# Optimization experiments

Measured on AMD Instinct MI355X. Metric: run time of the kernel, lower is better.

## Reference

```python
import jax, jax.numpy as jnp
import numpy as np

HEADS = 4

def setup_inputs() -> dict:
    B, L, D = 4, 2048, 256
    key = jax.random.key(0)
    k1, k2, k3, k4, k5, k6 = jax.random.split(key, 6)
    return {
        "atten": jax.random.normal(k1, (B, L, L), dtype=jnp.float32),
        "value": jax.random.normal(k2, (B, L, D), dtype=jnp.float32),
        "mask": jax.random.uniform(k3, (B, 1, L, L), dtype=jnp.float32),
        "padding_mask": jax.random.randint(k4, (B, L, L), 0, 2, dtype=jnp.int32),
        "Wv": jax.random.normal(k5, (D, D), dtype=jnp.float32) * 0.02,
        "bv": jnp.zeros((D,), dtype=jnp.float32),
        "Wo": jax.random.normal(k6, (D, D), dtype=jnp.float32) * 0.02,
        "bo": jnp.zeros((D,), dtype=jnp.float32),
    }

def reference(atten, value, mask, padding_mask, Wv, bv, Wo, bo):
    B, L, D = value.shape
    H = HEADS
    dk = D // H
    # to_value: Linear then split heads. N == 1 (value.unsqueeze(1) in torch).
    v = value @ Wv + bv                                   # (B, L, D)
    v = v.reshape(B, 1, L, H, dk).transpose(0, 3, 1, 2, 4)  # (B, H, N=1, L, dk)
    # externally supplied attention logits, two sequential masked fills
    a = atten[:, None, :, :]                              # (B, 1, L, L)
    a = jnp.where(mask < 0.5, jnp.finfo(a.dtype).min, a)
    a = jnp.where(padding_mask[:, None, :, :] == 0, -jnp.inf, a)
    a = jax.nn.softmax(a, axis=-1)                        # (B, 1, L, L)
    # dropout is identity in eval mode
    # einsum 'bhij,bhnjk->bhnik' with h=1 on a broadcast across H heads of v
    out = jnp.einsum('bij,bhnjk->bhnik', a[:, 0], v)      # (B, H, 1, L, dk)
    out = out.transpose(0, 2, 3, 1, 4).reshape(B, 1, L, D)
    out = out @ Wo + bo                                   # (B, 1, L, D)
    return out
```

## Files before the change

### kernel.cpp

```cpp
#include <hip/hip_runtime.h>
#include <hip/hip_bf16.h>
#include <math.h>

#define L 2048
#define D 256

typedef __attribute__((ext_vector_type(8))) short bf16x8;
typedef __attribute__((ext_vector_type(4))) float f32x4;
typedef __attribute__((ext_vector_type(4))) int i32x4;

__device__ __forceinline__ unsigned short f2bf(float f) {
    union { float f; unsigned int u; } v; v.f = f;
    unsigned int r = v.u + 0x7FFFu + ((v.u >> 16) & 1u);
    return (unsigned short)(r >> 16);
}

__global__ __launch_bounds__(256) void wtrans_kernel(
    const float* __restrict__ Wv, const float* __restrict__ Wo,
    unsigned short* __restrict__ Wvt, unsigned short* __restrict__ Wot) {
    int idx = blockIdx.x * 256 + threadIdx.x;
    int which = idx >> 16;
    int e = idx & 65535;
    int n = e >> 8, k = e & 255;
    const float* W = which ? Wo : Wv;
    unsigned short* Wt = which ? Wot : Wvt;
    Wt[n * 256 + k] = f2bf(W[k * 256 + n]);
}

__global__ __launch_bounds__(256) void gemm_v_kernel(
    const float* __restrict__ A,
    const unsigned short* __restrict__ Wt,
    const float* __restrict__ bias,
    unsigned short* __restrict__ Vt) {
    const int wave = threadIdx.x >> 6;
    const int lane = threadIdx.x & 63;
    const int mh = wave >> 1, nh = wave & 1;
    const int lm = lane & 15, q = lane >> 4;
    const int m0 = blockIdx.x * 64;
    const int n0 = blockIdx.y * 128;

    f32x4 acc[2][4];
#pragma unroll
    for (int i = 0; i < 2; i++)
#pragma unroll
        for (int j = 0; j < 4; j++) acc[i][j] = (f32x4)(0.f);

    int arow[2];
    arow[0] = m0 + mh * 32 + lm;
    arow[1] = arow[0] + 16;
    int ncol[4];
#pragma unroll
    for (int nf = 0; nf < 4; nf++) ncol[nf] = n0 + nh * 64 + nf * 16 + lm;

    for (int k0 = 0; k0 < 256; k0 += 32) {
        int kq = k0 + q * 8;
        bf16x8 bfr[4];
#pragma unroll
        for (int nf = 0; nf < 4; nf++)
            bfr[nf] = *reinterpret_cast<const bf16x8*>(Wt + ncol[nf] * 256 + kq);
        bf16x8 afr[2];
#pragma unroll
        for (int mf = 0; mf < 2; mf++) {
            const float* ap = A + arow[mf] * 256 + kq;
            f32x4 a0 = *reinterpret_cast<const f32x4*>(ap);
            f32x4 a1 = *reinterpret_cast<const f32x4*>(ap + 4);
            bf16x8 t;
#pragma unroll
            for (int e = 0; e < 4; e++) t[e] = (short)f2bf(a0[e]);
#pragma unroll
            for (int e = 0; e < 4; e++) t[4 + e] = (short)f2bf(a1[e]);
            afr[mf] = t;
        }
#pragma unroll
        for (int mf = 0; mf < 2; mf++)
#pragma unroll
            for (int nf = 0; nf < 4; nf++)
                acc[mf][nf] = __builtin_amdgcn_mfma_f32_16x16x32_bf16(
                    afr[mf], bfr[nf], acc[mf][nf], 0, 0, 0);
    }

#pragma unroll
    for (int mf = 0; mf < 2; mf++) {
        int mrow = m0 + mh * 32 + mf * 16 + q * 4;
#pragma unroll
        for (int nf = 0; nf < 4; nf++) {
            int n = ncol[nf];
            float bias_n = bias[n];
            int b = mrow >> 11;
            int j = mrow & 2047;
            unsigned short* dst = Vt + (size_t)b * (D * L) + (size_t)n * L + j;
            ushort4 pk;
            pk.x = f2bf(acc[mf][nf][0] + bias_n);
            pk.y = f2bf(acc[mf][nf][1] + bias_n);
            pk.z = f2bf(acc[mf][nf][2] + bias_n);
            pk.w = f2bf(acc[mf][nf][3] + bias_n);
            *reinterpret_cast<ushort4*>(dst) = pk;
        }
    }
}

__global__ __launch_bounds__(256) void p_kernel(
    const float* __restrict__ atten, const float* __restrict__ mask,
    const int* __restrict__ pad, unsigned short* __restrict__ P,
    float* __restrict__ lsum) {
    const int row = blockIdx.x * 4 + (threadIdx.x >> 6);
    const int lane = threadIdx.x & 63;

    const float* at = atten + (size_t)row * L;
    const float* mk = mask  + (size_t)row * L;
    const int*   pd = pad   + (size_t)row * L;
    unsigned short* Pr = P + (size_t)row * L;

    float l_th = 0.f;
#pragma unroll
    for (int c = 0; c < 8; c++) {
        const int off = c * 256 + lane * 4;
        f32x4 a = *reinterpret_cast<const f32x4*>(at + off);
        f32x4 m = *reinterpret_cast<const f32x4*>(mk + off);
        i32x4 p = *reinterpret_cast<const i32x4*>(pd + off);
        ushort4 pk;
        float pv;
        pv = (m[0] < 0.5f || p[0] == 0) ? 0.f : __expf(a[0]); l_th += pv; pk.x = f2bf(pv);
        pv = (m[1] < 0.5f || p[1] == 0) ? 0.f : __expf(a[1]); l_th += pv; pk.y = f2bf(pv);
        pv = (m[2] < 0.5f || p[2] == 0) ? 0.f : __expf(a[2]); l_th += pv; pk.z = f2bf(pv);
        pv = (m[3] < 0.5f || p[3] == 0) ? 0.f : __expf(a[3]); l_th += pv; pk.w = f2bf(pv);
        *reinterpret_cast<ushort4*>(Pr + off) = pk;
    }
#pragma unroll
    for (int off = 1; off < 64; off <<= 1) l_th += __shfl_xor(l_th, off);
    if (lane == 0) lsum[row] = l_th;
}

__global__ __launch_bounds__(256) void pv_out_kernel(
    const unsigned short* __restrict__ P, const unsigned short* __restrict__ Vt,
    const float* __restrict__ lsum, const unsigned short* __restrict__ Wot,
    const float* __restrict__ bo, float* __restrict__ out) {
    const int rb = blockIdx.x;
    const int tid = threadIdx.x;
    const int w = tid >> 6, lane = tid & 63;
    const int lm = lane & 15, q = lane >> 4;
    const int b = rb >> 6;
    const int row0 = rb * 32;

    const unsigned short* pA = P + (size_t)row0 * L + q * 8;
    const unsigned short* pB = Vt + (size_t)b * (D * L) + (size_t)(w * 64) * L + q * 8;

    f32x4 acc[2][4];
#pragma unroll
    for (int i = 0; i < 2; i++)
#pragma unroll
        for (int j = 0; j < 4; j++) acc[i][j] = (f32x4)(0.f);

    bf16x8 Ac[2][2], Bc[2][4], An[2][2], Bn[2][4];
#pragma unroll
    for (int kk = 0; kk < 2; kk++) {
#pragma unroll
        for (int mf = 0; mf < 2; mf++)
            Ac[kk][mf] = *reinterpret_cast<const bf16x8*>(pA + (mf * 16 + lm) * L + kk * 32);
#pragma unroll
        for (int nf = 0; nf < 4; nf++)
            Bc[kk][nf] = *reinterpret_cast<const bf16x8*>(pB + (nf * 16 + lm) * L + kk * 32);
    }

    for (int k0 = 0; k0 < 2048; k0 += 64) {
        if (k0 + 64 < 2048) {
            const int kn = k0 + 64;
#pragma unroll
            for (int kk = 0; kk < 2; kk++) {
#pragma unroll
                for (int mf = 0; mf < 2; mf++)
                    An[kk][mf] = *reinterpret_cast<const bf16x8*>(
                        pA + (mf * 16 + lm) * L + kn + kk * 32);
#pragma unroll
                for (int nf = 0; nf < 4; nf++)
                    Bn[kk][nf] = *reinterpret_cast<const bf16x8*>(
                        pB + (nf * 16 + lm) * L + kn + kk * 32);
            }
        }
#pragma unroll
        for (int kk = 0; kk < 2; kk++)
#pragma unroll
            for (int mf = 0; mf < 2; mf++)
#pragma unroll
                for (int nf = 0; nf < 4; nf++)
                    acc[mf][nf] = __builtin_amdgcn_mfma_f32_16x16x32_bf16(
                        Ac[kk][mf], Bc[kk][nf], acc[mf][nf], 0, 0, 0);
#pragma unroll
        for (int kk = 0; kk < 2; kk++) {
#pragma unroll
            for (int mf = 0; mf < 2; mf++) Ac[kk][mf] = An[kk][mf];
#pragma unroll
            for (int nf = 0; nf < 4; nf++) Bc[kk][nf] = Bn[kk][nf];
        }
    }

    __shared__ __align__(16) unsigned short Alds[32][264];
#pragma unroll
    for (int mf = 0; mf < 2; mf++) {
        float inv[4];
#pragma unroll
        for (int rg = 0; rg < 4; rg++)
            inv[rg] = 1.f / lsum[row0 + mf * 16 + q * 4 + rg];
#pragma unroll
        for (int nf = 0; nf < 4; nf++) {
            int col = w * 64 + nf * 16 + lm;
#pragma unroll
            for (int rg = 0; rg < 4; rg++)
                Alds[mf * 16 + q * 4 + rg][col] = f2bf(acc[mf][nf][rg] * inv[rg]);
        }
    }
    __syncthreads();

    f32x4 oacc[2][4];
#pragma unroll
    for (int i = 0; i < 2; i++)
#pragma unroll
        for (int j = 0; j < 4; j++) oacc[i][j] = (f32x4)(0.f);
    int ncol[4];
#pragma unroll
    for (int nf = 0; nf < 4; nf++) ncol[nf] = w * 64 + nf * 16 + lm;

    for (int kk = 0; kk < 8; kk++) {
        int kq = kk * 32 + q * 8;
        bf16x8 bfr[4];
#pragma unroll
        for (int nf = 0; nf < 4; nf++)
            bfr[nf] = *reinterpret_cast<const bf16x8*>(Wot + ncol[nf] * 256 + kq);
#pragma unroll
        for (int mf = 0; mf < 2; mf++) {
            bf16x8 afr = *reinterpret_cast<const bf16x8*>(&Alds[mf * 16 + lm][kq]);
#pragma unroll
            for (int nf = 0; nf < 4; nf++)
                oacc[mf][nf] = __builtin_amdgcn_mfma_f32_16x16x32_bf16(
                    afr, bfr[nf], oacc[mf][nf], 0, 0, 0);
        }
    }

#pragma unroll
    for (int mf = 0; mf < 2; mf++) {
        int mrow = row0 + mf * 16 + q * 4;
#pragma unroll
        for (int nf = 0; nf < 4; nf++) {
            int n = ncol[nf];
            float bn = bo[n];
#pragma unroll
            for (int rg = 0; rg < 4; rg++)
                out[(size_t)(mrow + rg) * 256 + n] = oacc[mf][nf][rg] + bn;
        }
    }
}

extern "C" void kernel_launch(void* const* d_in, const int* in_sizes, int n_in,
                              void* d_out, int out_size, void* d_ws, size_t ws_size,
                              hipStream_t stream) {
    (void)in_sizes; (void)n_in; (void)out_size; (void)ws_size;
    const float* atten = (const float*)d_in[0];
    const float* value = (const float*)d_in[1];
    const float* mask  = (const float*)d_in[2];
    const int*   pad   = (const int*)d_in[3];
    const float* Wv    = (const float*)d_in[4];
    const float* bv    = (const float*)d_in[5];
    const float* Wo    = (const float*)d_in[6];
    const float* bo    = (const float*)d_in[7];
    float* out = (float*)d_out;

    char* ws = (char*)d_ws;
    unsigned short* Vt  = (unsigned short*)(ws);
    unsigned short* Wvt = (unsigned short*)(ws + 4194304);
    unsigned short* Wot = (unsigned short*)(ws + 4325376);
    unsigned short* P   = (unsigned short*)(ws + 4456448);
    float* lsum         = (float*)(ws + 38010880);

    wtrans_kernel<<<512, 256, 0, stream>>>(Wv, Wo, Wvt, Wot);
    gemm_v_kernel<<<dim3(128, 2), 256, 0, stream>>>(value, Wvt, bv, Vt);
    p_kernel<<<2048, 256, 0, stream>>>(atten, mask, pad, P, lsum);
    pv_out_kernel<<<256, 256, 0, stream>>>(P, Vt, lsum, Wot, bo, out);
}
```

Before: 279.5 us.

## Split PV matmul over K into partial sums with separate combine+output GEMM

The P·V kernel is split four ways along the key dimension, so 1024 blocks run instead of 256. Each block writes fp32 partial sums to workspace, and a new combine kernel sums them, normalises by the row sums, and applies the Wo projection. The p_kernel now gives each wave half a row and prefetches the next chunk, producing two partial row sums. This trades better GPU occupancy for an extra kernel launch and roughly 32MB of partial-sum traffic through global memory.

```diff
diff --git a/kernel.cpp b/kernel.cpp
--- a/kernel.cpp
+++ b/kernel.cpp
@@ -102,48 +102,59 @@
 __global__ __launch_bounds__(256) void p_kernel(
     const float* __restrict__ atten, const float* __restrict__ mask,
     const int* __restrict__ pad, unsigned short* __restrict__ P,
-    float* __restrict__ lsum) {
-    const int row = blockIdx.x * 4 + (threadIdx.x >> 6);
+    float* __restrict__ lsum2) {
+    const int wid = blockIdx.x * 4 + (threadIdx.x >> 6);
+    const int row = wid >> 1, h = wid & 1;
     const int lane = threadIdx.x & 63;
 
-    const float* at = atten + (size_t)row * L;
-    const float* mk = mask  + (size_t)row * L;
-    const int*   pd = pad   + (size_t)row * L;
-    unsigned short* Pr = P + (size_t)row * L;
+    const size_t base = (size_t)row * L + h * 1024 + lane * 4;
+    const float* at = atten + base;
+    const float* mk = mask  + base;
+    const int*   pd = pad   + base;
+    unsigned short* Pr = P + base;
+
+    f32x4 a0 = *reinterpret_cast<const f32x4*>(at);
+    f32x4 m0 = *reinterpret_cast<const f32x4*>(mk);
+    i32x4 p0 = *reinterpret_cast<const i32x4*>(pd);
 
     float l_th = 0.f;
 #pragma unroll
-    for (int c = 0; c < 8; c++) {
-        const int off = c * 256 + lane * 4;
-        f32x4 a = *reinterpret_cast<const f32x4*>(at + off);
-        f32x4 m = *reinterpret_cast<const f32x4*>(mk + off);
-        i32x4 p = *reinterpret_cast<const i32x4*>(pd + off);
+    for (int c = 0; c < 4; c++) {
+        f32x4 a1, m1; i32x4 p1;
+        if (c < 3) {
+            const int off = (c + 1) * 256;
+            a1 = *reinterpret_cast<const f32x4*>(at + off);
+            m1 = *reinterpret_cast<const f32x4*>(mk + off);
+            p1 = *reinterpret_cast<const i32x4*>(pd + off);
+        }
         ushort4 pk;
         float pv;
-        pv = (m[0] < 0.5f || p[0] == 0) ? 0.f : __expf(a[0]); l_th += pv; pk.x = f2bf(pv);
-        pv = (m[1] < 0.5f || p[1] == 0) ? 0.f : __expf(a[1]); l_th += pv; pk.y = f2bf(pv);
-        pv = (m[2] < 0.5f || p[2] == 0) ? 0.f : __expf(a[2]); l_th += pv; pk.z = f2bf(pv);
-        pv = (m[3] < 0.5f || p[3] == 0) ? 0.f : __expf(a[3]); l_th += pv; pk.w = f2bf(pv);
-        *reinterpret_cast<ushort4*>(Pr + off) = pk;
+        pv = (m0[0] < 0.5f || p0[0] == 0) ? 0.f : __expf(a0[0]); l_th += pv; pk.x = f2bf(pv);
+        pv = (m0[1] < 0.5f || p0[1] == 0) ? 0.f : __expf(a0[1]); l_th += pv; pk.y = f2bf(pv);
+        pv = (m0[2] < 0.5f || p0[2] == 0) ? 0.f : __expf(a0[2]); l_th += pv; pk.z = f2bf(pv);
+        pv = (m0[3] < 0.5f || p0[3] == 0) ? 0.f : __expf(a0[3]); l_th += pv; pk.w = f2bf(pv);
+        *reinterpret_cast<ushort4*>(Pr + c * 256) = pk;
+        a0 = a1; m0 = m1; p0 = p1;
     }
 #pragma unroll
     for (int off = 1; off < 64; off <<= 1) l_th += __shfl_xor(l_th, off);
-    if (lane == 0) lsum[row] = l_th;
-}
-
-__global__ __launch_bounds__(256) void pv_out_kernel(
+    if (lane == 0) lsum2[wid] = l_th;
+}
+
+__global__ __launch_bounds__(256) void pv_split_kernel(
     const unsigned short* __restrict__ P, const unsigned short* __restrict__ Vt,
-    const float* __restrict__ lsum, const unsigned short* __restrict__ Wot,
-    const float* __restrict__ bo, float* __restrict__ out) {
+    float* __restrict__ part) {
     const int rb = blockIdx.x;
+    const int sk = blockIdx.y;
     const int tid = threadIdx.x;
     const int w = tid >> 6, lane = tid & 63;
     const int lm = lane & 15, q = lane >> 4;
     const int b = rb >> 6;
     const int row0 = rb * 32;
 
-    const unsigned short* pA = P + (size_t)row0 * L + q * 8;
-    const unsigned short* pB = Vt + (size_t)b * (D * L) + (size_t)(w * 64) * L + q * 8;
+    const unsigned short* pA = P + (size_t)row0 * L + sk * 512 + q * 8;
+    const unsigned short* pB = Vt + (size_t)b * (D * L) + (size_t)(w * 64) * L
+                             + sk * 512 + q * 8;
 
     f32x4 acc[2][4];
 #pragma unroll
@@ -151,71 +162,85 @@
 #pragma unroll
         for (int j = 0; j < 4; j++) acc[i][j] = (f32x4)(0.f);
 
-    bf16x8 Ac[2][2], Bc[2][4], An[2][2], Bn[2][4];
-#pragma unroll
-    for (int kk = 0; kk < 2; kk++) {
+    bf16x8 Ac[2], Bc[4], An[2], Bn[4];
+#pragma unroll
+    for (int mf = 0; mf < 2; mf++)
+        Ac[mf] = *reinterpret_cast<const bf16x8*>(pA + (mf * 16 + lm) * L);
+#pragma unroll
+    for (int nf = 0; nf < 4; nf++)
+        Bc[nf] = *reinterpret_cast<const bf16x8*>(pB + (nf * 16 + lm) * L);
+
+    for (int t = 0; t < 16; t++) {
+        if (t < 15) {
+            const int kn = (t + 1) * 32;
+#pragma unroll
+            for (int mf = 0; mf < 2; mf++)
+                An[mf] = *reinterpret_cast<const bf16x8*>(pA + (mf * 16 + lm) * L + kn);
+#pragma unroll
+            for (int nf = 0; nf < 4; nf++)
+                Bn[nf] = *reinterpret_cast<const bf16x8*>(pB + (nf * 16 + lm) * L + kn);
+        }
 #pragma unroll
         for (int mf = 0; mf < 2; mf++)
-            Ac[kk][mf] = *reinterpret_cast<const bf16x8*>(pA + (mf * 16 + lm) * L + kk * 32);
-#pragma unroll
-        for (int nf = 0; nf < 4; nf++)
-            Bc[kk][nf] = *reinterpret_cast<const bf16x8*>(pB + (nf * 16 + lm) * L + kk * 32);
-    }
-
-    for (int k0 = 0; k0 < 2048; k0 += 64) {
-        if (k0 + 64 < 2048) {
-            const int kn = k0 + 64;
-#pragma unroll
-            for (int kk = 0; kk < 2; kk++) {
-#pragma unroll
-                for (int mf = 0; mf < 2; mf++)
-                    An[kk][mf] = *reinterpret_cast<const bf16x8*>(
-                        pA + (mf * 16 + lm) * L + kn + kk * 32);
-#pragma unroll
-                for (int nf = 0; nf < 4; nf++)
-                    Bn[kk][nf] = *reinterpret_cast<const bf16x8*>(
-                        pB + (nf * 16 + lm) * L + kn + kk * 32);
-            }
-        }
-#pragma unroll
-        for (int kk = 0; kk < 2; kk++)
-#pragma unroll
-            for (int mf = 0; mf < 2; mf++)
-#pragma unroll
-                for (int nf = 0; nf < 4; nf++)
-                    acc[mf][nf] = __builtin_amdgcn_mfma_f32_16x16x32_bf16(
-                        Ac[kk][mf], Bc[kk][nf], acc[mf][nf], 0, 0, 0);
-#pragma unroll
-        for (int kk = 0; kk < 2; kk++) {
-#pragma unroll
-            for (int mf = 0; mf < 2; mf++) Ac[kk][mf] = An[kk][mf];
-#pragma unroll
-            for (int nf = 0; nf < 4; nf++) Bc[kk][nf] = Bn[kk][nf];
-        }
-    }
-
-    __shared__ __align__(16) unsigned short Alds[32][264];
-#pragma unroll
-    for (int mf = 0; mf < 2; mf++) {
-        float inv[4];
-#pragma unroll
-        for (int rg = 0; rg < 4; rg++)
-            inv[rg] = 1.f / lsum[row0 + mf * 16 + q * 4 + rg];
+#pragma unroll
+            for (int nf = 0; nf < 4; nf++)
+                acc[mf][nf] = __builtin_amdgcn_mfma_f32_16x16x32_bf16(
+                    Ac[mf], Bc[nf], acc[mf][nf], 0, 0, 0);
+#pragma unroll
+        for (int mf = 0; mf < 2; mf++) Ac[mf] = An[mf];
+#pragma unroll
+        for (int nf = 0; nf < 4; nf++) Bc[nf] = Bn[nf];
+    }
+
+    float* pb = part + ((size_t)sk * 256 + rb) * (32 * 256);
+#pragma unroll
+    for (int mf = 0; mf < 2; mf++)
 #pragma unroll
         for (int nf = 0; nf < 4; nf++) {
             int col = w * 64 + nf * 16 + lm;
 #pragma unroll
             for (int rg = 0; rg < 4; rg++)
-                Alds[mf * 16 + q * 4 + rg][col] = f2bf(acc[mf][nf][rg] * inv[rg]);
+                pb[(mf * 16 + q * 4 + rg) * 256 + col] = acc[mf][nf][rg];
+        }
+}
+
+__global__ __launch_bounds__(256) void combine_gemm_kernel(
+    const float* __restrict__ part, const float* __restrict__ lsum2,
+    const unsigned short* __restrict__ Wot, const float* __restrict__ bo,
+    float* __restrict__ out) {
+    const int cb = blockIdx.x;
+    const int tid = threadIdx.x;
+    const int w = tid >> 6, lane = tid & 63;
+    const int lm = lane & 15, q = lane >> 4;
+    const int rb = cb >> 1;
+    const int rlo = (cb & 1) * 16;
+
+    __shared__ __align__(16) unsigned short Alds[16][264];
+
+    {
+        const int r16 = tid >> 4;
+        const int c0 = (tid & 15) * 16;
+        const int g = cb * 16 + r16;
+        float l = lsum2[2 * g] + lsum2[2 * g + 1];
+        float inv = 1.f / l;
+        const float* pb = part + (size_t)rb * (32 * 256) + (rlo + r16) * 256 + c0;
+#pragma unroll
+        for (int e = 0; e < 16; e += 4) {
+            f32x4 s = (f32x4)(0.f);
+#pragma unroll
+            for (int skp = 0; skp < 4; skp++)
+                s += *reinterpret_cast<const f32x4*>(pb + (size_t)skp * (256 * 32 * 256) + e);
+            s *= inv;
+            ushort4 pk;
+            pk.x = f2bf(s[0]); pk.y = f2bf(s[1]); pk.z = f2bf(s[2]); pk.w = f2bf(s[3]);
+            *reinterpret_cast<ushort4*>(&Alds[r16][c0 + e]) = pk;
         }
     }
     __syncthreads();
 
-    f32x4 oacc[2][4];
-#pragma unroll
-    for (int i = 0; i < 2; i++)
-#pragma unroll
-        for (int j = 0; j < 4; j++) oacc[i][j] = (f32x4)(0.f);
+    f32x4 oacc[4];
+#pragma unroll
+    for (int j = 0; j < 4; j++) oacc[j] = (f32x4)(0.f);
     int ncol[4];
 #pragma unroll
     for (int nf = 0; nf < 4; nf++) ncol[nf] = w * 64 + nf * 16 + lm;
@@ -226,27 +251,21 @@
 #pragma unroll
         for (int nf = 0; nf < 4; nf++)
             bfr[nf] = *reinterpret_cast<const bf16x8*>(Wot + ncol[nf] * 256 + kq);
-#pragma unroll
-        for (int mf = 0; mf < 2; mf++) {
-            bf16x8 afr = *reinterpret_cast<const bf16x8*>(&Alds[mf * 16 + lm][kq]);
-#pragma unroll
-            for (int nf = 0; nf < 4; nf++)
-                oacc[mf][nf] = __builtin_amdgcn_mfma_f32_16x16x32_bf16(
-                    afr, bfr[nf], oacc[mf][nf], 0, 0, 0);
-        }
-    }
-
-#pragma unroll
-    for (int mf = 0; mf < 2; mf++) {
-        int mrow = row0 + mf * 16 + q * 4;
-#pragma unroll
-        for (int nf = 0; nf < 4; nf++) {
-            int n = ncol[nf];
-            float bn = bo[n];
-#pragma unroll
-            for (int rg = 0; rg < 4; rg++)
-                out[(size_t)(mrow + rg) * 256 + n] = oacc[mf][nf][rg] + bn;
-        }
+        bf16x8 afr = *reinterpret_cast<const bf16x8*>(&Alds[lm][kq]);
+#pragma unroll
+        for (int nf = 0; nf < 4; nf++)
+            oacc[nf] = __builtin_amdgcn_mfma_f32_16x16x32_bf16(
+                afr, bfr[nf], oacc[nf], 0, 0, 0);
+    }
+
+    const int mrow = cb * 16 + q * 4;
+#pragma unroll
+    for (int nf = 0; nf < 4; nf++) {
+        int n = ncol[nf];
+        float bn = bo[n];
+#pragma unroll
+        for (int rg = 0; rg < 4; rg++)
+            out[(size_t)(mrow + rg) * 256 + n] = oacc[nf][rg] + bn;
     }
 }
 
@@ -269,10 +288,12 @@
     unsigned short* Wvt = (unsigned short*)(ws + 4194304);
     unsigned short* Wot = (unsigned short*)(ws + 4325376);
     unsigned short* P   = (unsigned short*)(ws + 4456448);
-    float* lsum         = (float*)(ws + 38010880);
+    float* lsum2        = (float*)(ws + 38010880);
+    float* part         = (float*)(ws + 38076416);
 
     wtrans_kernel<<<512, 256, 0, stream>>>(Wv, Wo, Wvt, Wot);
     gemm_v_kernel<<<dim3(128, 2), 256, 0, stream>>>(value, Wvt, bv, Vt);
-    p_kernel<<<2048, 256, 0, stream>>>(atten, mask, pad, P, lsum);
-    pv_out_kernel<<<256, 256, 0, stream>>>(P, Vt, lsum, Wot, bo, out);
-}
+    p_kernel<<<4096, 256, 0, stream>>>(atten, mask, pad, P, lsum2);
+    pv_split_kernel<<<dim3(256, 4), 256, 0, stream>>>(P, Vt, part);
+    combine_gemm_kernel<<<512, 256, 0, stream>>>(part, lsum2, Wot, bo, out);
+}
```

Result: slower. 289.2 us (+3.4%).
